# Kernel tuning notes

Measured on AMD Instinct MI355X. Metric: run time of the kernel, lower is better.

Reference implementation:

```python
import jax, jax.numpy as jnp
import numpy as np

N_POI = 50000
D = 128
E = 400000
GCN_NUM = 3
HEADS = 8
B = 64
L = 100
LEAKY_SLOPE = 0.01
NORM_EPS = 1e-12


def setup_inputs() -> dict:
    key = jax.random.key(0)
    ks = jax.random.split(key, 11)
    return {
        "embeds": jax.random.normal(ks[0], (N_POI, D), jnp.float32) * 0.1,
        "gcn_W": jax.random.normal(ks[1], (GCN_NUM, D, D), jnp.float32) * (1.0 / np.sqrt(D)),
        "gcn_b": jnp.zeros((GCN_NUM, D), jnp.float32),
        "in_proj_w": jax.random.normal(ks[2], (3 * D, D), jnp.float32) * (1.0 / np.sqrt(D)),
        "in_proj_b": jnp.zeros((3 * D,), jnp.float32),
        "out_proj_w": jax.random.normal(ks[3], (D, D), jnp.float32) * (1.0 / np.sqrt(D)),
        "out_proj_b": jnp.zeros((D,), jnp.float32),
        "dist_vec": jax.random.uniform(ks[4], (E,), jnp.float32),
        "dist_edges": jax.random.randint(ks[5], (2, E), 0, N_POI),
        "x_idx": jax.random.randint(ks[6], (B * L,), 0, N_POI),
        "poi_idx": jax.random.randint(ks[7], (B,), 0, N_POI),
    }


def _self_attn(x, in_w, in_b, out_w, out_b):
    # x: [B, L, D]; standard nn.MultiheadAttention with Q=K=V=x, batch_first
    b, l, d = x.shape
    hd = d // HEADS
    qkv = x @ in_w.T + in_b                      # [B, L, 3D]
    q, k, v = jnp.split(qkv, 3, axis=-1)
    def heads(t):
        return t.reshape(b, l, HEADS, hd).transpose(0, 2, 1, 3)  # [B, H, L, hd]
    q, k, v = heads(q), heads(k), heads(v)
    scores = jnp.einsum('bhqd,bhkd->bhqk', q, k) / jnp.sqrt(jnp.asarray(hd, x.dtype))
    attn = jax.nn.softmax(scores, axis=-1)
    o = jnp.einsum('bhqk,bhkd->bhqd', attn, v).transpose(0, 2, 1, 3).reshape(b, l, d)
    return o @ out_w.T + out_b


def reference(embeds, gcn_W, gcn_b, in_proj_w, in_proj_b, out_proj_w, out_proj_b,
              dist_vec, dist_edges, x_idx, poi_idx):
    n_poi = embeds.shape[0]
    loop = jnp.arange(n_poi)
    # symmetrize edges + add self-loops (done in GeoGraph.__init__)
    rows = jnp.concatenate([dist_edges[0], dist_edges[1], loop])
    cols = jnp.concatenate([dist_edges[1], dist_edges[0], loop])
    dv = jnp.concatenate([dist_vec, dist_vec, jnp.zeros((n_poi,), dist_vec.dtype)])
    # symmetric degree normalization over destination (col) index
    deg = jax.ops.segment_sum(jnp.ones_like(dv), cols, num_segments=n_poi)
    dis = jnp.where(deg > 0, jax.lax.rsqrt(jnp.maximum(deg, 1e-12)), 0.0)
    w = jnp.exp(-dv ** 2) * dis[rows] * dis[cols]   # [E_full]

    enc = embeds
    for i in range(GCN_NUM):
        # sparse.mm: out[row] += w * enc[col]
        agg = jax.ops.segment_sum(w[:, None] * enc[cols], rows, num_segments=n_poi)
        enc = agg @ gcn_W[i].T + gcn_b[i]
        enc = jax.nn.leaky_relu(enc, LEAKY_SLOPE)
        enc = enc / jnp.maximum(jnp.linalg.norm(enc, axis=-1, keepdims=True), NORM_EPS)

    tar_embed = enc[poi_idx]                         # [B, D]
    geo_feat = enc[x_idx].reshape(B, L, D)           # equal-length sessions -> pad is a reshape
    attn_out = _self_attn(geo_feat, in_proj_w, in_proj_b, out_proj_w, out_proj_b)
    aggr_feat = attn_out.mean(axis=1)                # [B, D]
    return aggr_feat, tar_embed
```

## Files before the change

### kernel.cpp

```cpp
#include <hip/hip_runtime.h>
#include <math.h>

#define D 128
#define GCN_NUM 3
#define HEADS 8
#define HD 16
#define L_SEQ 100
#define LEAKY 0.01f
#define SC_BUCKETS 8

typedef __attribute__((ext_vector_type(8))) short short8v;
typedef __attribute__((ext_vector_type(4))) float f32x4;

__device__ __forceinline__ unsigned f2bf(float x) {
  unsigned u = __float_as_uint(x);
  return (u + 0x7FFFu + ((u >> 16) & 1u)) >> 16;
}
__device__ __forceinline__ float bflo2f(unsigned u) { return __uint_as_float(u << 16); }
__device__ __forceinline__ float bfhi2f(unsigned u) { return __uint_as_float(u & 0xFFFF0000u); }


__global__ void convert3(const float* __restrict__ s0, unsigned short* __restrict__ d0, int n0,
                         const float* __restrict__ s1, unsigned short* __restrict__ d1, int n1,
                         const float* __restrict__ s2, unsigned short* __restrict__ d2, int n2) {
  int i = blockIdx.x * blockDim.x + threadIdx.x;
  const float* s; unsigned short* d; int j;
  if (i < n0)            { s = s0; d = d0; j = i; }
  else if (i < n0 + n1)  { s = s1; d = d1; j = i - n0; }
  else if (i < n0 + n1 + n2) { s = s2; d = d2; j = i - n0 - n1; }
  else return;
  float4 v = reinterpret_cast<const float4*>(s)[j];
  uint2 o;
  o.x = f2bf(v.x) | (f2bf(v.y) << 16);
  o.y = f2bf(v.z) | (f2bf(v.w) << 16);
  reinterpret_cast<uint2*>(d)[j] = o;
}


__global__ void fill_deg(int* __restrict__ deg, int n) {
  int i = blockIdx.x * blockDim.x + threadIdx.x;
  if (i < n) deg[i] = 1;
}

__global__ void count_deg(const int* __restrict__ e0, const int* __restrict__ e1,
                          int* __restrict__ deg, int E) {
  int stride = gridDim.x * blockDim.x;
  for (int i = blockIdx.x * blockDim.x + threadIdx.x; i < E; i += stride) {
    atomicAdd(&deg[e0[i]], 1);
    atomicAdd(&deg[e1[i]], 1);
  }
}


__global__ __launch_bounds__(1024) void block_sum(const int* __restrict__ deg,
                                                  int* __restrict__ bsum, int n) {
  __shared__ int ws[16];
  int tid = threadIdx.x, lane = tid & 63, wid = tid >> 6;
  int i = blockIdx.x * 1024 + tid;
  int v = (i < n) ? deg[i] : 0;
#pragma unroll
  for (int off = 32; off; off >>= 1) v += __shfl_xor(v, off);
  if (lane == 0) ws[wid] = v;
  __syncthreads();
  if (tid == 0) {
    int s = 0;
#pragma unroll
    for (int k = 0; k < 16; ++k) s += ws[k];
    bsum[blockIdx.x] = s;
  }
}

__global__ __launch_bounds__(1024) void scan_final(
    const int* __restrict__ deg, const int* __restrict__ bsum,
    int* __restrict__ row_ptr, int* __restrict__ cursor, int n, int nb) {
  __shared__ int ws[16];
  __shared__ int prefix_s;
  int tid = threadIdx.x, lane = tid & 63, wid = tid >> 6;
  int i = blockIdx.x * 1024 + tid;
  int v = (i < n) ? deg[i] : 0;
  int x = v;
#pragma unroll
  for (int off = 1; off < 64; off <<= 1) {
    int y = __shfl_up(x, off);
    if (lane >= off) x += y;
  }
  if (lane == 63) ws[wid] = x;
  __syncthreads();
  if (wid == 0) {
    int pv = (lane < blockIdx.x) ? bsum[lane] : 0;
#pragma unroll
    for (int off = 32; off; off >>= 1) pv += __shfl_xor(pv, off);
    if (lane == 0) prefix_s = pv;
    int s = (lane < 16) ? ws[lane] : 0;
#pragma unroll
    for (int off = 1; off < 16; off <<= 1) {
      int y = __shfl_up(s, off);
      if (lane >= off) s += y;
    }
    if (lane < 16) ws[lane] = s;
  }
  __syncthreads();
  int woff = wid ? ws[wid - 1] : 0;
  int prefix = prefix_s;
  if (i < n) {
    int pval = prefix + woff + (x - v);
    row_ptr[i] = pval;
    cursor[i] = pval;
  }
  if (blockIdx.x == nb - 1 && tid == 0) row_ptr[n] = prefix + ws[15];
}

__global__ __launch_bounds__(256) void scatter_edges_b(
    const int* __restrict__ e0, const int* __restrict__ e1,
    const float* __restrict__ dv, const int* __restrict__ deg,
    int* __restrict__ cursor, uint2* __restrict__ ecw,
    int E, int N, int span, int bpb) {
  int bucket = blockIdx.x / bpb;
  int bx = blockIdx.x % bpb;
  int rlo = bucket * span;
  int rhi = min(rlo + span, N);
  int total = 2 * E + N;
  int stride = bpb * 256;
  for (int i = bx * 256 + threadIdx.x; i < total; i += stride) {
    int r, c; bool self = false;
    if (i < E)          { r = e0[i];     c = e1[i]; }
    else if (i < 2 * E) { r = e1[i - E]; c = e0[i - E]; }
    else                { r = i - 2 * E; c = r; self = true; }
    if (r < rlo || r >= rhi) continue;
    float d = self ? 0.f : dv[(i < E) ? i : i - E];
    float w = expf(-d * d) * (1.0f / sqrtf((float)deg[r])) * (1.0f / sqrtf((float)deg[c]));
    int pos = atomicAdd(&cursor[r], 1);
    ecw[pos] = make_uint2((unsigned)c, __float_as_uint(w));
  }
}


__global__ __launch_bounds__(256) void spmm_bf(
    const int* __restrict__ row_ptr, const uint2* __restrict__ ecw,
    const unsigned short* __restrict__ enc, unsigned short* __restrict__ agg, int n) {
  int r = blockIdx.x * 4 + (threadIdx.x >> 6);
  if (r >= n) return;
  int lane = threadIdx.x & 63;
  int g = lane >> 4, t = lane & 15;
  int s = row_ptr[r], e = row_ptr[r + 1];
  float a0 = 0.f, a1 = 0.f, a2 = 0.f, a3 = 0.f, a4 = 0.f, a5 = 0.f, a6 = 0.f, a7 = 0.f;
  int i = s + g;
  uint2 cwA = make_uint2(0u, 0u), cwB = make_uint2(0u, 0u);
  if (i < e) cwA = ecw[i];
  if (i + 4 < e) cwB = ecw[i + 4];
  while (i + 4 < e) {
    uint2 cwC = cwA, cwD = cwB;
    if (i + 8 < e)  cwC = ecw[i + 8];
    if (i + 12 < e) cwD = ecw[i + 12];
    float wA = __uint_as_float(cwA.y), wB = __uint_as_float(cwB.y);
    uint4 uA = *reinterpret_cast<const uint4*>(enc + (size_t)cwA.x * D + t * 8);
    uint4 uB = *reinterpret_cast<const uint4*>(enc + (size_t)cwB.x * D + t * 8);
    a0 = fmaf(wA, bflo2f(uA.x), a0); a1 = fmaf(wA, bfhi2f(uA.x), a1);
    a2 = fmaf(wA, bflo2f(uA.y), a2); a3 = fmaf(wA, bfhi2f(uA.y), a3);
    a4 = fmaf(wA, bflo2f(uA.z), a4); a5 = fmaf(wA, bfhi2f(uA.z), a5);
    a6 = fmaf(wA, bflo2f(uA.w), a6); a7 = fmaf(wA, bfhi2f(uA.w), a7);
    a0 = fmaf(wB, bflo2f(uB.x), a0); a1 = fmaf(wB, bfhi2f(uB.x), a1);
    a2 = fmaf(wB, bflo2f(uB.y), a2); a3 = fmaf(wB, bfhi2f(uB.y), a3);
    a4 = fmaf(wB, bflo2f(uB.z), a4); a5 = fmaf(wB, bfhi2f(uB.z), a5);
    a6 = fmaf(wB, bflo2f(uB.w), a6); a7 = fmaf(wB, bfhi2f(uB.w), a7);
    cwA = cwC; cwB = cwD;
    i += 8;
  }
  if (i < e) {
    float wA = __uint_as_float(cwA.y);
    uint4 uA = *reinterpret_cast<const uint4*>(enc + (size_t)cwA.x * D + t * 8);
    a0 = fmaf(wA, bflo2f(uA.x), a0); a1 = fmaf(wA, bfhi2f(uA.x), a1);
    a2 = fmaf(wA, bflo2f(uA.y), a2); a3 = fmaf(wA, bfhi2f(uA.y), a3);
    a4 = fmaf(wA, bflo2f(uA.z), a4); a5 = fmaf(wA, bfhi2f(uA.z), a5);
    a6 = fmaf(wA, bflo2f(uA.w), a6); a7 = fmaf(wA, bfhi2f(uA.w), a7);
  }
  a0 += __shfl_xor(a0, 16); a0 += __shfl_xor(a0, 32);
  a1 += __shfl_xor(a1, 16); a1 += __shfl_xor(a1, 32);
  a2 += __shfl_xor(a2, 16); a2 += __shfl_xor(a2, 32);
  a3 += __shfl_xor(a3, 16); a3 += __shfl_xor(a3, 32);
  a4 += __shfl_xor(a4, 16); a4 += __shfl_xor(a4, 32);
  a5 += __shfl_xor(a5, 16); a5 += __shfl_xor(a5, 32);
  a6 += __shfl_xor(a6, 16); a6 += __shfl_xor(a6, 32);
  a7 += __shfl_xor(a7, 16); a7 += __shfl_xor(a7, 32);
  if (g == 0) {
    uint4 o;
    o.x = f2bf(a0) | (f2bf(a1) << 16);
    o.y = f2bf(a2) | (f2bf(a3) << 16);
    o.z = f2bf(a4) | (f2bf(a5) << 16);
    o.w = f2bf(a6) | (f2bf(a7) << 16);
    *reinterpret_cast<uint4*>(agg + (size_t)r * D + t * 8) = o;
  }
}

__global__ __launch_bounds__(256) void dense_mfma(
    const unsigned short* __restrict__ A, const unsigned short* __restrict__ Wb,
    const float* __restrict__ bias, unsigned short* __restrict__ enc, int n) {
  __shared__ unsigned short Wl[128 * 136];
  int tid = threadIdx.x;
  {
    int cg = (tid & 15) * 8;
    int r0 = tid >> 4;
#pragma unroll
    for (int i = 0; i < 8; ++i) {
      int row = r0 + i * 16;
      *reinterpret_cast<short8v*>(&Wl[row * 136 + cg]) =
          *reinterpret_cast<const short8v*>(Wb + row * D + cg);
    }
  }
  __syncthreads();
  int w = tid >> 6, lane = tid & 63;
  int lr = lane & 15, lg = lane >> 4;
#pragma unroll
  for (int rt = 0; rt < 2; ++rt) {
    int rbase = blockIdx.x * 128 + rt * 64 + w * 16;
    f32x4 acc[8];
#pragma unroll
    for (int j = 0; j < 8; ++j) acc[j] = f32x4{0.f, 0.f, 0.f, 0.f};
    const unsigned short* arow = A + (size_t)(rbase + lr) * D + lg * 8;
#pragma unroll
    for (int ks = 0; ks < 4; ++ks) {
      short8v a = *reinterpret_cast<const short8v*>(arow + ks * 32);
#pragma unroll
      for (int jt = 0; jt < 8; ++jt) {
        short8v b = *reinterpret_cast<const short8v*>(&Wl[(jt * 16 + lr) * 136 + ks * 32 + lg * 8]);
        acc[jt] = __builtin_amdgcn_mfma_f32_16x16x32_bf16(a, b, acc[jt], 0, 0, 0);
      }
    }
    float vals[8][4];
    float ss[4] = {0.f, 0.f, 0.f, 0.f};
#pragma unroll
    for (int jt = 0; jt < 8; ++jt) {
      float bj = bias[jt * 16 + lr];
#pragma unroll
      for (int i = 0; i < 4; ++i) {
        float t = acc[jt][i] + bj;
        t = (t > 0.f) ? t : LEAKY * t;
        vals[jt][i] = t;
        ss[i] += t * t;
      }
    }
#pragma unroll
    for (int i = 0; i < 4; ++i) {
      float s = ss[i];
      s += __shfl_xor(s, 1); s += __shfl_xor(s, 2);
      s += __shfl_xor(s, 4); s += __shfl_xor(s, 8);
      ss[i] = 1.0f / fmaxf(sqrtf(s), 1e-12f);
    }
#pragma unroll
    for (int i = 0; i < 4; ++i) {
      int row = rbase + lg * 4 + i;
      if (row < n) {
#pragma unroll
        for (int jt = 0; jt < 8; ++jt)
          enc[(size_t)row * D + jt * 16 + lr] = (unsigned short)f2bf(vals[jt][i] * ss[i]);
      }
    }
  }
}


__global__ void gather_all(const unsigned short* __restrict__ src,
                           const int* __restrict__ x_idx, const int* __restrict__ poi_idx,
                           unsigned short* __restrict__ geo, float* __restrict__ tar,
                           int BL, int B) {
  int i = blockIdx.x;
  int t = threadIdx.x;
  if (i < BL) {
    reinterpret_cast<unsigned*>(geo + (size_t)i * D)[t] =
        reinterpret_cast<const unsigned*>(src + (size_t)x_idx[i] * D)[t];
  } else {
    int j = i - BL;
    unsigned u = reinterpret_cast<const unsigned*>(src + (size_t)poi_idx[j] * D)[t];
    reinterpret_cast<float2*>(tar + (size_t)j * D)[t] = make_float2(bflo2f(u), bfhi2f(u));
  }
}

__global__ __launch_bounds__(256) void qkv_mfma(
    const unsigned short* __restrict__ A, const unsigned short* __restrict__ Wb,
    const float* __restrict__ bias, float* __restrict__ qkv, int M) {
  __shared__ unsigned short Wl[128 * 136];
  int tid = threadIdx.x;
  const unsigned short* Wslab = Wb + (size_t)blockIdx.y * 128 * D;
  {
    int cg = (tid & 15) * 8;
    int r0 = tid >> 4;
#pragma unroll
    for (int i = 0; i < 8; ++i) {
      int row = r0 + i * 16;
      *reinterpret_cast<short8v*>(&Wl[row * 136 + cg]) =
          *reinterpret_cast<const short8v*>(Wslab + row * D + cg);
    }
  }
  __syncthreads();
  int w = tid >> 6, lane = tid & 63;
  int lr = lane & 15, lg = lane >> 4;
  int colbase = blockIdx.y * 128;
#pragma unroll
  for (int rt = 0; rt < 2; ++rt) {
    int rbase = blockIdx.x * 128 + rt * 64 + w * 16;
    f32x4 acc[8];
#pragma unroll
    for (int j = 0; j < 8; ++j) acc[j] = f32x4{0.f, 0.f, 0.f, 0.f};
    const unsigned short* arow = A + (size_t)(rbase + lr) * D + lg * 8;
#pragma unroll
    for (int ks = 0; ks < 4; ++ks) {
      short8v a = *reinterpret_cast<const short8v*>(arow + ks * 32);
#pragma unroll
      for (int jt = 0; jt < 8; ++jt) {
        short8v b = *reinterpret_cast<const short8v*>(&Wl[(jt * 16 + lr) * 136 + ks * 32 + lg * 8]);
        acc[jt] = __builtin_amdgcn_mfma_f32_16x16x32_bf16(a, b, acc[jt], 0, 0, 0);
      }
    }
#pragma unroll
    for (int jt = 0; jt < 8; ++jt) {
      int j = colbase + jt * 16 + lr;
      float bj = bias[j];
#pragma unroll
      for (int i = 0; i < 4; ++i) {
        int row = rbase + lg * 4 + i;
        if (row < M) qkv[(size_t)row * 384 + j] = acc[jt][i] + bj;
      }
    }
  }
}

__global__ __launch_bounds__(128) void attn_kernel(
    const float* __restrict__ qkv, float* __restrict__ o) {
  __shared__ float k_s[L_SEQ][HD];
  __shared__ float v_s[L_SEQ][HD];
  __shared__ float sc[L_SEQ][L_SEQ + 1];
  int b = blockIdx.x / HEADS;
  int h = blockIdx.x % HEADS;
  int tid = threadIdx.x;
  const size_t rowbase = (size_t)b * L_SEQ;
  for (int idx = tid; idx < L_SEQ * HD; idx += 128) {
    int l = idx >> 4, d2 = idx & 15;
    const float* base = qkv + (rowbase + l) * 384 + h * HD + d2;
    k_s[l][d2] = base[128];
    v_s[l][d2] = base[256];
  }
  __syncthreads();
  if (tid < L_SEQ) {
    float q[HD];
    const float* qp = qkv + (rowbase + tid) * 384 + h * HD;
#pragma unroll
    for (int d2 = 0; d2 < HD; ++d2) q[d2] = qp[d2];
    float m = -1e30f;
    for (int j = 0; j < L_SEQ; ++j) {
      float s = 0.f;
#pragma unroll
      for (int d2 = 0; d2 < HD; ++d2) s += q[d2] * k_s[j][d2];
      s *= 0.25f;
      sc[tid][j] = s;
      m = fmaxf(m, s);
    }
    float sum = 0.f;
    for (int j = 0; j < L_SEQ; ++j) {
      float e = expf(sc[tid][j] - m);
      sc[tid][j] = e;
      sum += e;
    }
    float inv = 1.f / sum;
    float oacc[HD];
#pragma unroll
    for (int d2 = 0; d2 < HD; ++d2) oacc[d2] = 0.f;
    for (int j = 0; j < L_SEQ; ++j) {
      float p = sc[tid][j];
#pragma unroll
      for (int d2 = 0; d2 < HD; ++d2) oacc[d2] += p * v_s[j][d2];
    }
    float* op = o + (rowbase + tid) * D + h * HD;
#pragma unroll
    for (int d2 = 0; d2 < HD; ++d2) op[d2] = oacc[d2] * inv;
  }
}

__global__ __launch_bounds__(128) void out_mean_kernel(
    const float* __restrict__ o, const float* __restrict__ Wo,
    const float* __restrict__ bo, float* __restrict__ out, int L) {
  __shared__ float m_s[D];
  int b = blockIdx.x, tid = threadIdx.x;
  float s = 0.f;
  for (int l = 0; l < L; ++l) s += o[((size_t)b * L + l) * D + tid];
  m_s[tid] = s / (float)L;
  __syncthreads();
  const float4* w4 = reinterpret_cast<const float4*>(Wo + (size_t)tid * D);
  float acc = 0.f;
  for (int k4 = 0; k4 < D / 4; ++k4) {
    float4 w = w4[k4];
    int k = k4 * 4;
    acc += m_s[k] * w.x + m_s[k + 1] * w.y + m_s[k + 2] * w.z + m_s[k + 3] * w.w;
  }
  out[(size_t)b * D + tid] = acc + bo[tid];
}


extern "C" void kernel_launch(void* const* d_in, const int* in_sizes, int n_in,
                              void* d_out, int out_size, void* d_ws, size_t ws_size,
                              hipStream_t stream) {
  const float* embeds   = (const float*)d_in[0];
  const float* gcn_W    = (const float*)d_in[1];
  const float* gcn_b    = (const float*)d_in[2];
  const float* in_w     = (const float*)d_in[3];
  const float* in_b     = (const float*)d_in[4];
  const float* out_w    = (const float*)d_in[5];
  const float* out_b    = (const float*)d_in[6];
  const float* dist_vec = (const float*)d_in[7];
  const int*   edges    = (const int*)d_in[8];
  const int*   x_idx    = (const int*)d_in[9];
  const int*   poi_idx  = (const int*)d_in[10];
  float* out = (float*)d_out;

  int N  = in_sizes[0] / D;
  int E  = in_sizes[7];
  int BL = in_sizes[9];
  int B  = in_sizes[10];
  int L  = BL / B;
  const int* e0 = edges;
  const int* e1 = edges + E;
  size_t total_edges = (size_t)2 * E + N;
  int Npad = ((N + 127) / 128) * 128;
  int NB   = (N + 1023) / 1024;

  char* p = (char*)d_ws;
  auto alloc = [&](size_t bytes) { char* q = p; p += (bytes + 255) & ~(size_t)255; return q; };
  int*   deg     = (int*)alloc((size_t)N * 4);
  int*   row_ptr = (int*)alloc((size_t)(N + 1) * 4);
  int*   cursor  = (int*)alloc((size_t)N * 4);
  int*   bsum    = (int*)alloc((size_t)NB * 4);
  uint2* ecw     = (uint2*)alloc(total_edges * 8);
  unsigned short* emb_bf = (unsigned short*)alloc((size_t)Npad * D * 2);
  unsigned short* W_bf   = (unsigned short*)alloc((size_t)GCN_NUM * D * D * 2);
  unsigned short* inw_bf = (unsigned short*)alloc((size_t)3 * D * D * 2);
  unsigned short* agg_bf = (unsigned short*)alloc((size_t)Npad * D * 2);
  unsigned short* enc_bf = (unsigned short*)alloc((size_t)Npad * D * 2);
  unsigned short* geo_bf = (unsigned short*)alloc((size_t)BL * D * 2);
  float* qkv  = (float*)alloc((size_t)BL * 384 * 4);
  float* obuf = (float*)alloc((size_t)BL * D * 4);

  int n4e = N * D / 4, n4w = GCN_NUM * D * D / 4, n4i = 3 * D * D / 4;
  int n4tot = n4e + n4w + n4i;
  convert3<<<(n4tot + 255) / 256, 256, 0, stream>>>(
      embeds, emb_bf, n4e, gcn_W, W_bf, n4w, in_w, inw_bf, n4i);

  fill_deg<<<(N + 255) / 256, 256, 0, stream>>>(deg, N);
  count_deg<<<1024, 256, 0, stream>>>(e0, e1, deg, E);
  block_sum<<<NB, 1024, 0, stream>>>(deg, bsum, N);
  scan_final<<<NB, 1024, 0, stream>>>(deg, bsum, row_ptr, cursor, N, NB);
  int span = (N + SC_BUCKETS - 1) / SC_BUCKETS;
  int bpb = 512;
  scatter_edges_b<<<SC_BUCKETS * bpb, 256, 0, stream>>>(
      e0, e1, dist_vec, deg, cursor, ecw, E, N, span, bpb);

  const unsigned short* cur_in = emb_bf;
  for (int i = 0; i < GCN_NUM; ++i) {
    spmm_bf<<<(N + 3) / 4, 256, 0, stream>>>(row_ptr, ecw, cur_in, agg_bf, N);
    dense_mfma<<<Npad / 128, 256, 0, stream>>>(
        agg_bf, W_bf + (size_t)i * D * D, gcn_b + (size_t)i * D, enc_bf, N);
    cur_in = enc_bf;
  }

  gather_all<<<BL + B, 64, 0, stream>>>(enc_bf, x_idx, poi_idx, geo_bf,
                                        out + (size_t)B * D, BL, B);
  dim3 qgrid(BL / 128, 3);
  qkv_mfma<<<qgrid, 256, 0, stream>>>(geo_bf, inw_bf, in_b, qkv, BL);
  attn_kernel<<<B * HEADS, 128, 0, stream>>>(qkv, obuf);
  out_mean_kernel<<<B, 128, 0, stream>>>(obuf, out_w, out_b, out, L);
}
```

Before: 370.1 us.

## Fuse degree init into convert, gather inside QKV GEMM, interleave scatter buckets

The degree-fill kernel is merged into the bf16 conversion kernel, and the session-row gather is folded into the QKV MFMA kernel, which now reads encoder rows through x_idx. Only the target-embedding gather stays a separate kernel. The edge scatter now interleaves bucket assignment across block indices, so blocks with adjacent indices work on different row ranges. This removes two launches and an intermediate geo buffer, at the cost of indirect A-row loads in the GEMM and a changed scatter access pattern.

```diff
diff --git a/kernel.cpp b/kernel.cpp
--- a/kernel.cpp
+++ b/kernel.cpp
@@ -20,27 +20,27 @@
 __device__ __forceinline__ float bfhi2f(unsigned u) { return __uint_as_float(u & 0xFFFF0000u); }
 
 
-__global__ void convert3(const float* __restrict__ s0, unsigned short* __restrict__ d0, int n0,
-                         const float* __restrict__ s1, unsigned short* __restrict__ d1, int n1,
-                         const float* __restrict__ s2, unsigned short* __restrict__ d2, int n2) {
+__global__ void prep(const float* __restrict__ s0, unsigned short* __restrict__ d0, int n0,
+                     const float* __restrict__ s1, unsigned short* __restrict__ d1, int n1,
+                     const float* __restrict__ s2, unsigned short* __restrict__ d2, int n2,
+                     int* __restrict__ deg, int N) {
   int i = blockIdx.x * blockDim.x + threadIdx.x;
-  const float* s; unsigned short* d; int j;
-  if (i < n0)            { s = s0; d = d0; j = i; }
-  else if (i < n0 + n1)  { s = s1; d = d1; j = i - n0; }
-  else if (i < n0 + n1 + n2) { s = s2; d = d2; j = i - n0 - n1; }
-  else return;
-  float4 v = reinterpret_cast<const float4*>(s)[j];
-  uint2 o;
-  o.x = f2bf(v.x) | (f2bf(v.y) << 16);
-  o.y = f2bf(v.z) | (f2bf(v.w) << 16);
-  reinterpret_cast<uint2*>(d)[j] = o;
-}
-
-
-__global__ void fill_deg(int* __restrict__ deg, int n) {
-  int i = blockIdx.x * blockDim.x + threadIdx.x;
-  if (i < n) deg[i] = 1;
-}
+  int n4tot = n0 + n1 + n2;
+  if (i < n4tot) {
+    const float* s; unsigned short* d; int j;
+    if (i < n0)           { s = s0; d = d0; j = i; }
+    else if (i < n0 + n1) { s = s1; d = d1; j = i - n0; }
+    else                  { s = s2; d = d2; j = i - n0 - n1; }
+    float4 v = reinterpret_cast<const float4*>(s)[j];
+    uint2 o;
+    o.x = f2bf(v.x) | (f2bf(v.y) << 16);
+    o.y = f2bf(v.z) | (f2bf(v.w) << 16);
+    reinterpret_cast<uint2*>(d)[j] = o;
+  } else if (i - n4tot < N) {
+    deg[i - n4tot] = 1;
+  }
+}
+
 
 __global__ void count_deg(const int* __restrict__ e0, const int* __restrict__ e1,
                           int* __restrict__ deg, int E) {
@@ -110,13 +110,13 @@
   if (blockIdx.x == nb - 1 && tid == 0) row_ptr[n] = prefix + ws[15];
 }
 
-__global__ __launch_bounds__(256) void scatter_edges_b(
+__global__ __launch_bounds__(256) void scatter_edges_x(
     const int* __restrict__ e0, const int* __restrict__ e1,
     const float* __restrict__ dv, const int* __restrict__ deg,
     int* __restrict__ cursor, uint2* __restrict__ ecw,
     int E, int N, int span, int bpb) {
-  int bucket = blockIdx.x / bpb;
-  int bx = blockIdx.x % bpb;
+  int bucket = blockIdx.x & (SC_BUCKETS - 1);
+  int bx = blockIdx.x >> 3;
   int rlo = bucket * span;
   int rhi = min(rlo + span, N);
   int total = 2 * E + N;
@@ -259,25 +259,20 @@
 }
 
 
-__global__ void gather_all(const unsigned short* __restrict__ src,
-                           const int* __restrict__ x_idx, const int* __restrict__ poi_idx,
-                           unsigned short* __restrict__ geo, float* __restrict__ tar,
-                           int BL, int B) {
-  int i = blockIdx.x;
-  int t = threadIdx.x;
-  if (i < BL) {
-    reinterpret_cast<unsigned*>(geo + (size_t)i * D)[t] =
-        reinterpret_cast<const unsigned*>(src + (size_t)x_idx[i] * D)[t];
-  } else {
-    int j = i - BL;
+__global__ void gather_tar(const unsigned short* __restrict__ src,
+                           const int* __restrict__ poi_idx, float* __restrict__ tar, int B) {
+  int j = blockIdx.x;
+  if (j < B) {
+    int t = threadIdx.x;
     unsigned u = reinterpret_cast<const unsigned*>(src + (size_t)poi_idx[j] * D)[t];
     reinterpret_cast<float2*>(tar + (size_t)j * D)[t] = make_float2(bflo2f(u), bfhi2f(u));
   }
 }
 
 __global__ __launch_bounds__(256) void qkv_mfma(
-    const unsigned short* __restrict__ A, const unsigned short* __restrict__ Wb,
-    const float* __restrict__ bias, float* __restrict__ qkv, int M) {
+    const unsigned short* __restrict__ enc, const int* __restrict__ x_idx,
+    const unsigned short* __restrict__ Wb, const float* __restrict__ bias,
+    float* __restrict__ qkv, int M) {
   __shared__ unsigned short Wl[128 * 136];
   int tid = threadIdx.x;
   const unsigned short* Wslab = Wb + (size_t)blockIdx.y * 128 * D;
@@ -301,7 +296,7 @@
     f32x4 acc[8];
 #pragma unroll
     for (int j = 0; j < 8; ++j) acc[j] = f32x4{0.f, 0.f, 0.f, 0.f};
-    const unsigned short* arow = A + (size_t)(rbase + lr) * D + lg * 8;
+    const unsigned short* arow = enc + (size_t)x_idx[rbase + lr] * D + lg * 8;
 #pragma unroll
     for (int ks = 0; ks < 4; ++ks) {
       short8v a = *reinterpret_cast<const short8v*>(arow + ks * 32);
@@ -434,22 +429,20 @@
   unsigned short* inw_bf = (unsigned short*)alloc((size_t)3 * D * D * 2);
   unsigned short* agg_bf = (unsigned short*)alloc((size_t)Npad * D * 2);
   unsigned short* enc_bf = (unsigned short*)alloc((size_t)Npad * D * 2);
-  unsigned short* geo_bf = (unsigned short*)alloc((size_t)BL * D * 2);
   float* qkv  = (float*)alloc((size_t)BL * 384 * 4);
   float* obuf = (float*)alloc((size_t)BL * D * 4);
 
   int n4e = N * D / 4, n4w = GCN_NUM * D * D / 4, n4i = 3 * D * D / 4;
-  int n4tot = n4e + n4w + n4i;
-  convert3<<<(n4tot + 255) / 256, 256, 0, stream>>>(
-      embeds, emb_bf, n4e, gcn_W, W_bf, n4w, in_w, inw_bf, n4i);
-
-  fill_deg<<<(N + 255) / 256, 256, 0, stream>>>(deg, N);
+  int prep_tot = n4e + n4w + n4i + N;
+  prep<<<(prep_tot + 255) / 256, 256, 0, stream>>>(
+      embeds, emb_bf, n4e, gcn_W, W_bf, n4w, in_w, inw_bf, n4i, deg, N);
+
   count_deg<<<1024, 256, 0, stream>>>(e0, e1, deg, E);
   block_sum<<<NB, 1024, 0, stream>>>(deg, bsum, N);
   scan_final<<<NB, 1024, 0, stream>>>(deg, bsum, row_ptr, cursor, N, NB);
   int span = (N + SC_BUCKETS - 1) / SC_BUCKETS;
   int bpb = 512;
-  scatter_edges_b<<<SC_BUCKETS * bpb, 256, 0, stream>>>(
+  scatter_edges_x<<<SC_BUCKETS * bpb, 256, 0, stream>>>(
       e0, e1, dist_vec, deg, cursor, ecw, E, N, span, bpb);
 
   const unsigned short* cur_in = emb_bf;
@@ -460,10 +453,9 @@
     cur_in = enc_bf;
   }
 
-  gather_all<<<BL + B, 64, 0, stream>>>(enc_bf, x_idx, poi_idx, geo_bf,
-                                        out + (size_t)B * D, BL, B);
+  gather_tar<<<B, 64, 0, stream>>>(enc_bf, poi_idx, out + (size_t)B * D, B);
   dim3 qgrid(BL / 128, 3);
-  qkv_mfma<<<qgrid, 256, 0, stream>>>(geo_bf, inw_bf, in_b, qkv, BL);
+  qkv_mfma<<<qgrid, 256, 0, stream>>>(enc_bf, x_idx, inw_bf, in_b, qkv, BL);
   attn_kernel<<<B * HEADS, 128, 0, stream>>>(qkv, obuf);
   out_mean_kernel<<<B, 128, 0, stream>>>(obuf, out_w, out_b, out, L);
 }
```

New measurement: 364.4 us. No clear change (-1.5%).
